# Kernel tuning notes

Hardware: AMD Instinct MI355X
Metric: run time of the kernel (lower is better)

The kernel has to match this reference:

```python
import jax, jax.numpy as jnp
import numpy as np

B_SZ, SEQ, IN, HID, MEM_D, ORDER = 64, 512, 512, 1024, 8, 256
THETA = 512.0


def _legendre_ab(order, theta):
    # Continuous-time Legendre delay system (Voelker et al.):
    # A[i,j] = (2i+1)/theta * (-1 if i<j else (-1)^(i-j+1));  B[i] = (2i+1)/theta * (-1)^i
    q = jnp.arange(order, dtype=jnp.float32)
    r = (2.0 * q + 1.0) / theta
    i, j = jnp.meshgrid(q, q, indexing='ij')
    a = jnp.where(i < j, -1.0, jnp.where(((i - j) % 2) == 1, 1.0, -1.0)) * r[:, None]
    b = jnp.where((q % 2) == 0, 1.0, -1.0) * r
    # ZOH discretization with dt=1 via augmented matrix exponential
    M = jnp.zeros((order + 1, order + 1), dtype=jnp.float32)
    M = M.at[:order, :order].set(a).at[:order, order].set(b)
    Md = jax.scipy.linalg.expm(M)
    return Md[:order, :order], Md[:order, order]


def setup_inputs() -> dict:
    key = jax.random.key(0)
    ks = jax.random.split(key, 7)
    def n(k, shape, s):
        return jax.random.normal(k, shape, dtype=jnp.float32) * jnp.float32(s)
    return {
        'x':   n(ks[0], (B_SZ, SEQ, IN), 1.0),
        'e_x': n(ks[1], (MEM_D, IN), 1.0 / np.sqrt(IN)),          # lecun_uniform_-like scale
        'e_h': n(ks[2], (MEM_D, HID), 1.0 / np.sqrt(HID)),
        'e_m': jnp.zeros((MEM_D, MEM_D * ORDER), dtype=jnp.float32),  # init_em = zeros_
        'W_x': n(ks[4], (HID, IN), np.sqrt(2.0 / (HID + IN))),    # xavier_normal_
        'W_h': n(ks[5], (HID, HID), np.sqrt(2.0 / (HID + HID))),
        'W_m': n(ks[6], (HID, MEM_D * ORDER), np.sqrt(2.0 / (HID + MEM_D * ORDER))),
    }


def reference(x, e_x, e_h, e_m, W_x, W_h, W_m):
    A, Bv = _legendre_ab(ORDER, THETA)
    bsz = x.shape[0]

    def step(carry, x_t):
        h, m = carry                      # h: [B,HID], m: [B,MEM_D,ORDER]
        m_flat = m.reshape(bsz, -1)
        # u_t = e_x x_t + e_h h_{t-1} + e_m m_{t-1}  -> [B, MEM_D]
        u = x_t @ e_x.T + h @ e_h.T + m_flat @ e_m.T
        # m_t = A m_{t-1} + B u_t (per memory channel)
        m = jnp.einsum('bdo,po->bdp', m, A) + u[:, :, None] * Bv
        m_flat = m.reshape(bsz, -1)
        # h_t = tanh(W_x x_t + W_h h_{t-1} + W_m m_t)
        h = jnp.tanh(x_t @ W_x.T + h @ W_h.T + m_flat @ W_m.T)
        return (h, m), h

    h0 = jnp.zeros((bsz, HID), dtype=x.dtype)
    m0 = jnp.zeros((bsz, MEM_D, ORDER), dtype=x.dtype)
    (_, _), ys = jax.lax.scan(step, (h0, m0), jnp.swapaxes(x, 0, 1))
    return jnp.swapaxes(ys, 0, 1)          # [B, SEQ, HID]
```

## Files before the change

### kernel.cpp

```cpp
#include <hip/hip_runtime.h>
#include <cmath>
#include <vector>

#define B_SZ 64
#define SEQ 512
#define IN_D 512
#define HID 1024
#define MEM_DIM 8
#define ORD 256
#define MFLAT 2048
#define KTOT 3584
#define NH 128
#define NM 64
#define NBLK (NH + NM)

typedef __attribute__((ext_vector_type(8))) short short8v;
typedef __attribute__((ext_vector_type(4))) float f32x4;

__device__ __host__ inline unsigned short f2bf(float f) {
  union { float f; unsigned u; } v; v.f = f;
  unsigned r = v.u + 0x7FFF + ((v.u >> 16) & 1);
  return (unsigned short)(r >> 16);
}
__device__ __host__ inline float bf2f(unsigned short h) {
  union { unsigned u; float f; } v; v.u = ((unsigned)h) << 16;
  return v.f;
}

static void matmul_d(const double* A, const double* B, double* C, int n) {
  for (int i = 0; i < n; ++i) {
    double* Ci = C + (size_t)i * n;
    for (int j = 0; j < n; ++j) Ci[j] = 0.0;
    const double* Ai = A + (size_t)i * n;
    for (int k = 0; k < n; ++k) {
      double a = Ai[k];
      const double* Bk = B + (size_t)k * n;
      for (int j = 0; j < n; ++j) Ci[j] += a * Bk[j];
    }
  }
}

static void compute_AB_host(float* AdT, float* Anat, float* Bd) {
  const int q = ORD, n = ORD + 1;
  const double theta = 512.0;
  std::vector<double> M((size_t)n * n, 0.0);
  for (int i = 0; i < q; ++i) {
    double r = (2.0 * i + 1.0) / theta;
    for (int j = 0; j < q; ++j) {
      double v = (i < j) ? -1.0 : ((((i - j) % 2) == 1) ? 1.0 : -1.0);
      M[(size_t)i * n + j] = v * r;
    }
    M[(size_t)i * n + q] = (((i % 2) == 0) ? 1.0 : -1.0) * r;
  }
  double norm = 0.0;
  for (int j = 0; j < n; ++j) {
    double s = 0.0;
    for (int i = 0; i < n; ++i) s += fabs(M[(size_t)i * n + j]);
    if (s > norm) norm = s;
  }
  int s = 0;
  while (norm > 0.25) { norm *= 0.5; ++s; }
  double sc = ldexp(1.0, -s);
  for (size_t i = 0; i < M.size(); ++i) M[i] *= sc;
  std::vector<double> E((size_t)n * n, 0.0), P = M, T((size_t)n * n);
  for (int i = 0; i < n; ++i) E[(size_t)i * n + i] = 1.0;
  for (size_t i = 0; i < M.size(); ++i) E[i] += M[i];
  for (int k = 2; k <= 30; ++k) {
    matmul_d(P.data(), M.data(), T.data(), n);
    double inv = 1.0 / (double)k, mx = 0.0;
    for (size_t i = 0; i < T.size(); ++i) {
      T[i] *= inv;
      double a = fabs(T[i]);
      if (a > mx) mx = a;
    }
    P.swap(T);
    for (size_t i = 0; i < M.size(); ++i) E[i] += P[i];
    if (mx < 1e-19) break;
  }
  for (int it = 0; it < s; ++it) {
    matmul_d(E.data(), E.data(), T.data(), n);
    E.swap(T);
  }
  for (int p = 0; p < q; ++p) {
    for (int o = 0; o < q; ++o) {
      float v = (float)E[(size_t)p * n + o];
      AdT[(size_t)o * q + p] = v;
      Anat[(size_t)p * q + o] = v;
    }
    Bd[p] = (float)E[(size_t)p * n + q];
  }
}

__global__ __launch_bounds__(256) void k_wmb(const float* __restrict__ Wm,
                                             const float* __restrict__ Bd,
                                             float* __restrict__ WmB) {
  int i = blockIdx.x;
  int d = threadIdx.x >> 5, l = threadIdx.x & 31;
  const float* wr = Wm + (size_t)i * MFLAT + d * ORD;
  float acc = 0.f;
  #pragma unroll
  for (int j = 0; j < 8; ++j) { int p = l + 32 * j; acc += wr[p] * Bd[p]; }
  for (int off = 16; off; off >>= 1) acc += __shfl_xor(acc, off);
  if (l == 0) WmB[i * 8 + d] = acc;
}

__global__ __launch_bounds__(256) void k_gcat(
    const float* __restrict__ Wx, const float* __restrict__ Wh,
    const float* __restrict__ Wm, const float* __restrict__ Ex,
    const float* __restrict__ Eh, const float* __restrict__ Em,
    const float* __restrict__ Anat, const float* __restrict__ WmB,
    unsigned short* __restrict__ Ghi, unsigned short* __restrict__ Glo) {
  __shared__ float wm[MFLAT];
  __shared__ float wb[8];
  int i = blockIdx.x, tid = threadIdx.x;
  for (int k = tid; k < MFLAT; k += 256) wm[k] = Wm[(size_t)i * MFLAT + k];
  if (tid < 8) wb[tid] = WmB[i * 8 + tid];
  __syncthreads();
  unsigned short* grh = Ghi + (size_t)i * KTOT;
  unsigned short* grl = Glo + (size_t)i * KTOT;
  for (int c = tid; c < KTOT; c += 256) {
    float v;
    if (c < IN_D) {
      v = Wx[(size_t)i * IN_D + c];
      #pragma unroll
      for (int d = 0; d < 8; ++d) v += wb[d] * Ex[(size_t)d * IN_D + c];
    } else if (c < IN_D + HID) {
      int j = c - IN_D;
      v = Wh[(size_t)i * HID + j];
      #pragma unroll
      for (int d = 0; d < 8; ++d) v += wb[d] * Eh[(size_t)d * HID + j];
    } else {
      int cm = c - IN_D - HID;
      int dd = cm >> 8, o = cm & 255;
      v = 0.f;
      const float* wmd = wm + dd * ORD;
      for (int p = 0; p < ORD; ++p) v += wmd[p] * Anat[(size_t)p * ORD + o];
      #pragma unroll
      for (int d = 0; d < 8; ++d) v += wb[d] * Em[(size_t)d * MFLAT + cm];
    }
    unsigned short hi = f2bf(v);
    grh[c] = hi;
    grl[c] = f2bf(v - bf2f(hi));
  }
}

__device__ inline void grid_barrier(unsigned* cnt, unsigned target) {
  __syncthreads();
  if (threadIdx.x == 0) {
    __hip_atomic_fetch_add(cnt, 1u, __ATOMIC_RELEASE, __HIP_MEMORY_SCOPE_AGENT);
    while (__hip_atomic_load(cnt, __ATOMIC_RELAXED, __HIP_MEMORY_SCOPE_AGENT) < target)
      __builtin_amdgcn_s_sleep(1);
    __builtin_amdgcn_fence(__ATOMIC_ACQUIRE, "agent");
  }
  __syncthreads();
}

__global__ __launch_bounds__(256) void k_persist(
    const float* __restrict__ x, const float* __restrict__ Ex,
    const float* __restrict__ Eh, const float* __restrict__ Em,
    const unsigned short* __restrict__ Ghi, const unsigned short* __restrict__ Glo,
    const float* __restrict__ AdT, const float* __restrict__ Bd,
    unsigned short* __restrict__ sh0, unsigned short* __restrict__ sh1,
    unsigned short* __restrict__ sl0, unsigned short* __restrict__ sl1,
    float* __restrict__ hfp0, float* __restrict__ hfp1,
    float* __restrict__ mfp0, float* __restrict__ mfp1,
    float* __restrict__ out, unsigned* __restrict__ cnt) {
  int tid = threadIdx.x;
  unsigned ep = 0;

  if (blockIdx.x < NH) {
    __shared__ float hx[2][64][4];
    int it = blockIdx.x & 63, bh = blockIdx.x >> 6;
    int w = tid >> 6, lane = tid & 63;
    int tw = w & 1, kh = w >> 1;
    int b0 = bh * 32 + tw * 16;
    int i0 = it * 16;
    size_t aoff = (size_t)(b0 + (lane & 15)) * KTOT + (lane >> 4) * 8;
    const unsigned short* bh_ = Ghi + (size_t)(i0 + (lane & 15)) * KTOT + (lane >> 4) * 8;
    const unsigned short* bl_ = Glo + (size_t)(i0 + (lane & 15)) * KTOT + (lane >> 4) * 8;

    grid_barrier(cnt, (++ep) * NBLK);

    for (int t = 0; t < SEQ; ++t) {
      const unsigned short* ah_ = ((t & 1) ? sh1 : sh0) + aoff;
      const unsigned short* al_ = ((t & 1) ? sl1 : sl0) + aoff;
      unsigned short* snh = (t & 1) ? sh0 : sh1;
      unsigned short* snl = (t & 1) ? sl0 : sl1;
      float* hn = (t & 1) ? hfp0 : hfp1;

      f32x4 ahh = {0.f,0.f,0.f,0.f}, alh = {0.f,0.f,0.f,0.f}, ahl = {0.f,0.f,0.f,0.f};
      int kbase = kh * 1792;
      #pragma unroll 4
      for (int kk = 0; kk < 56; ++kk) {
        int k = kbase + kk * 32;
        short8v avh = *(const short8v*)(ah_ + k);
        short8v avl = *(const short8v*)(al_ + k);
        short8v bvh = *(const short8v*)(bh_ + k);
        short8v bvl = *(const short8v*)(bl_ + k);
        ahh = __builtin_amdgcn_mfma_f32_16x16x32_bf16(avh, bvh, ahh, 0, 0, 0);
        alh = __builtin_amdgcn_mfma_f32_16x16x32_bf16(avl, bvh, alh, 0, 0, 0);
        ahl = __builtin_amdgcn_mfma_f32_16x16x32_bf16(avh, bvl, ahl, 0, 0, 0);
      }
      f32x4 acc = ahh + alh + ahl;
      if (kh == 1) {
        *(f32x4*)&hx[tw][lane][0] = acc;
      }
      __syncthreads();
      if (kh == 0) {
        f32x4 o4 = *(const f32x4*)&hx[tw][lane][0];
        #pragma unroll
        for (int r = 0; r < 4; ++r) {
          float v = acc[r] + o4[r];
          float hv = tanhf(v);
          int b = b0 + (lane >> 4) * 4 + r;
          int i = i0 + (lane & 15);
          hn[(size_t)b * HID + i] = hv;
          unsigned short hi = f2bf(hv);
          snh[(size_t)b * KTOT + IN_D + i] = hi;
          snl[(size_t)b * KTOT + IN_D + i] = f2bf(hv - bf2f(hi));
          __builtin_nontemporal_store(hv, &out[((size_t)b * SEQ + t) * HID + i]);
        }
      }
      grid_barrier(cnt, (++ep) * NBLK);
    }
  } else {
    __shared__ float sst[KTOT];
    int b = blockIdx.x - NH;
    int d = tid >> 5, l = tid & 31;
    int p0 = l * 8;
    const float* exr = Ex + (size_t)d * IN_D;
    const float* ehr = Eh + (size_t)d * HID;
    const float* emr = Em + (size_t)d * MFLAT;
    float bdv[8];
    #pragma unroll
    for (int j = 0; j < 8; ++j) bdv[j] = Bd[p0 + j];

    {
      const float* xr = x + (size_t)b * SEQ * IN_D;
      for (int k = tid; k < IN_D; k += 256) {
        float xv = xr[k];
        unsigned short hi = f2bf(xv);
        sh0[(size_t)b * KTOT + k] = hi;
        sl0[(size_t)b * KTOT + k] = f2bf(xv - bf2f(hi));
      }
    }
    grid_barrier(cnt, (++ep) * NBLK);

    for (int t = 0; t < SEQ; ++t) {
      const float* hc = (t & 1) ? hfp1 : hfp0;
      const float* mc = (t & 1) ? mfp1 : mfp0;
      float* mn = (t & 1) ? mfp0 : mfp1;
      unsigned short* snh = (t & 1) ? sh0 : sh1;
      unsigned short* snl = (t & 1) ? sl0 : sl1;

      const float* xrow = x + ((size_t)b * SEQ + t) * IN_D;
      #pragma unroll
      for (int j = 0; j < 14; ++j) {
        int k = tid + 256 * j;
        float v;
        if (k < IN_D) v = xrow[k];
        else if (k < IN_D + HID) v = hc[(size_t)b * HID + (k - IN_D)];
        else v = mc[(size_t)b * MFLAT + (k - IN_D - HID)];
        sst[k] = v;
      }
      __syncthreads();

      float ua = 0.f;
      #pragma unroll 4
      for (int j = 0; j < 16; ++j) { int k = l + 32 * j; ua += exr[k] * sst[k]; }
      #pragma unroll 4
      for (int j = 0; j < 32; ++j) { int k = l + 32 * j; ua += ehr[k] * sst[IN_D + k]; }
      #pragma unroll 4
      for (int j = 0; j < 64; ++j) { int k = l + 32 * j; ua += emr[k] * sst[IN_D + HID + k]; }
      #pragma unroll
      for (int off = 16; off; off >>= 1) ua += __shfl_xor(ua, off);

      float a0 = bdv[0]*ua, a1 = bdv[1]*ua, a2 = bdv[2]*ua, a3 = bdv[3]*ua;
      float a4 = bdv[4]*ua, a5 = bdv[5]*ua, a6 = bdv[6]*ua, a7 = bdv[7]*ua;
      const float* mrow = sst + IN_D + HID + d * ORD;
      #pragma unroll 4
      for (int o = 0; o < ORD; ++o) {
        float mv = mrow[o];
        const float4* aq = (const float4*)(AdT + (size_t)o * ORD + p0);
        float4 q0 = aq[0], q1 = aq[1];
        a0 = fmaf(q0.x, mv, a0); a1 = fmaf(q0.y, mv, a1);
        a2 = fmaf(q0.z, mv, a2); a3 = fmaf(q0.w, mv, a3);
        a4 = fmaf(q1.x, mv, a4); a5 = fmaf(q1.y, mv, a5);
        a6 = fmaf(q1.z, mv, a6); a7 = fmaf(q1.w, mv, a7);
      }
      float4* mo4 = (float4*)(mn + (size_t)b * MFLAT + d * ORD + p0);
      mo4[0] = make_float4(a0, a1, a2, a3);
      mo4[1] = make_float4(a4, a5, a6, a7);
      float av[8] = { a0, a1, a2, a3, a4, a5, a6, a7 };
      unsigned short ph[8], pl[8];
      #pragma unroll
      for (int j = 0; j < 8; ++j) {
        ph[j] = f2bf(av[j]);
        pl[j] = f2bf(av[j] - bf2f(ph[j]));
      }
      size_t moff = (size_t)b * KTOT + IN_D + HID + d * ORD + p0;
      *(short8v*)(snh + moff) = *(short8v*)ph;
      *(short8v*)(snl + moff) = *(short8v*)pl;

      if (t + 1 < SEQ) {
        const float* xn = x + ((size_t)b * SEQ + t + 1) * IN_D;
        for (int k = tid; k < IN_D; k += 256) {
          float xv = xn[k];
          unsigned short hi = f2bf(xv);
          snh[(size_t)b * KTOT + k] = hi;
          snl[(size_t)b * KTOT + k] = f2bf(xv - bf2f(hi));
        }
      }
      __syncthreads();
      grid_barrier(cnt, (++ep) * NBLK);
    }
  }
}

extern "C" void kernel_launch(void* const* d_in, const int* in_sizes, int n_in,
                              void* d_out, int out_size, void* d_ws, size_t ws_size,
                              hipStream_t stream) {
  const float* x  = (const float*)d_in[0];
  const float* Ex = (const float*)d_in[1];
  const float* Eh = (const float*)d_in[2];
  const float* Em = (const float*)d_in[3];
  const float* Wx = (const float*)d_in[4];
  const float* Wh = (const float*)d_in[5];
  const float* Wm = (const float*)d_in[6];
  float* out = (float*)d_out;
  float* ws = (float*)d_ws;

  float* dAnat = ws;
  float* dAdT  = dAnat + 65536;
  float* dBd   = dAdT + 65536;
  float* dWmB  = dBd + 512;
  unsigned short* dGhi = (unsigned short*)(dWmB + 8192);
  unsigned short* dGlo = dGhi + (size_t)HID * KTOT;
  unsigned short* sh0  = dGlo + (size_t)HID * KTOT;
  unsigned short* sh1  = sh0 + (size_t)B_SZ * KTOT;
  unsigned short* sl0  = sh1 + (size_t)B_SZ * KTOT;
  unsigned short* sl1  = sl0 + (size_t)B_SZ * KTOT;
  float* hfp0 = (float*)(sl1 + (size_t)B_SZ * KTOT);
  float* hfp1 = hfp0 + B_SZ * HID;
  float* mfp0 = hfp1 + B_SZ * HID;
  float* mfp1 = mfp0 + B_SZ * MFLAT;
  unsigned* dCnt = (unsigned*)(mfp1 + B_SZ * MFLAT);

  static float h_AdT[ORD * ORD];
  static float h_Anat[ORD * ORD];
  static float h_Bd[ORD];
  compute_AB_host(h_AdT, h_Anat, h_Bd);
  hipMemcpyAsync(dAdT,  h_AdT,  sizeof(h_AdT),  hipMemcpyHostToDevice, stream);
  hipMemcpyAsync(dAnat, h_Anat, sizeof(h_Anat), hipMemcpyHostToDevice, stream);
  hipMemcpyAsync(dBd,   h_Bd,   sizeof(h_Bd),   hipMemcpyHostToDevice, stream);

  hipMemsetAsync(sh0, 0, (size_t)B_SZ * KTOT * sizeof(unsigned short), stream);
  hipMemsetAsync(sl0, 0, (size_t)B_SZ * KTOT * sizeof(unsigned short), stream);
  hipMemsetAsync(hfp0, 0, (size_t)B_SZ * HID * sizeof(float), stream);
  hipMemsetAsync(mfp0, 0, (size_t)B_SZ * MFLAT * sizeof(float), stream);
  hipMemsetAsync(dCnt, 0, sizeof(unsigned), stream);

  k_wmb<<<dim3(HID), dim3(256), 0, stream>>>(Wm, dBd, dWmB);
  k_gcat<<<dim3(HID), dim3(256), 0, stream>>>(Wx, Wh, Wm, Ex, Eh, Em, dAnat, dWmB, dGhi, dGlo);

  k_persist<<<dim3(NBLK), dim3(256), 0, stream>>>(
      x, Ex, Eh, Em, dGhi, dGlo, dAdT, dBd, sh0, sh1, sl0, sl1,
      hfp0, hfp1, mfp0, mfp1, out, dCnt);
}
```

Before: 21.12 ms.

## Replace atomic-counter grid barrier with flag-array barrier and restructure memory update

Swaps the single atomic-counter grid barrier for a centralized scheme. Each block writes its epoch to its own padded flag slot, block 0 polls all the slots, and it then releases everyone through one go flag, so blocks no longer contend on one atomic. The memory-update blocks also change how they compute A·m. Each thread now covers all 8 memory channels for 4 outputs over a quarter of the order dimension, so every AdT element loaded is reused 8 times, and the partial sums are reduced through shared memory. The added cost is extra shared memory, more syncthreads, and a serial poll in block 0 on every step.

```diff
diff --git a/kernel.cpp b/kernel.cpp
--- a/kernel.cpp
+++ b/kernel.cpp
@@ -13,6 +13,7 @@
 #define NH 128
 #define NM 64
 #define NBLK (NH + NM)
+#define BAR_STRIDE 16
 
 typedef __attribute__((ext_vector_type(8))) short short8v;
 typedef __attribute__((ext_vector_type(4))) float f32x4;
@@ -144,14 +145,28 @@
   }
 }
 
-__device__ inline void grid_barrier(unsigned* cnt, unsigned target) {
+__device__ inline void grid_barrier(unsigned* __restrict__ arr,
+                                    unsigned* __restrict__ go, unsigned ep) {
   __syncthreads();
-  if (threadIdx.x == 0) {
-    __hip_atomic_fetch_add(cnt, 1u, __ATOMIC_RELEASE, __HIP_MEMORY_SCOPE_AGENT);
-    while (__hip_atomic_load(cnt, __ATOMIC_RELAXED, __HIP_MEMORY_SCOPE_AGENT) < target)
-      __builtin_amdgcn_s_sleep(1);
+  if (blockIdx.x == 0) {
+    int tid = threadIdx.x;
+    if (tid > 0 && tid < NBLK) {
+      while (__hip_atomic_load(&arr[tid * BAR_STRIDE], __ATOMIC_RELAXED,
+                               __HIP_MEMORY_SCOPE_AGENT) < ep) {}
+    }
+    __syncthreads();
+    if (tid == 0)
+      __hip_atomic_store(go, ep, __ATOMIC_RELEASE, __HIP_MEMORY_SCOPE_AGENT);
+  } else {
+    if (threadIdx.x == 0) {
+      __hip_atomic_store(&arr[blockIdx.x * BAR_STRIDE], ep, __ATOMIC_RELEASE,
+                         __HIP_MEMORY_SCOPE_AGENT);
+      while (__hip_atomic_load(go, __ATOMIC_RELAXED,
+                               __HIP_MEMORY_SCOPE_AGENT) < ep) {}
+    }
+  }
+  if (threadIdx.x == 0)
     __builtin_amdgcn_fence(__ATOMIC_ACQUIRE, "agent");
-  }
   __syncthreads();
 }
 
@@ -164,7 +179,8 @@
     unsigned short* __restrict__ sl0, unsigned short* __restrict__ sl1,
     float* __restrict__ hfp0, float* __restrict__ hfp1,
     float* __restrict__ mfp0, float* __restrict__ mfp1,
-    float* __restrict__ out, unsigned* __restrict__ cnt) {
+    float* __restrict__ out, unsigned* __restrict__ barArr,
+    unsigned* __restrict__ barGo) {
   int tid = threadIdx.x;
   unsigned ep = 0;
 
@@ -179,7 +195,7 @@
     const unsigned short* bh_ = Ghi + (size_t)(i0 + (lane & 15)) * KTOT + (lane >> 4) * 8;
     const unsigned short* bl_ = Glo + (size_t)(i0 + (lane & 15)) * KTOT + (lane >> 4) * 8;
 
-    grid_barrier(cnt, (++ep) * NBLK);
+    grid_barrier(barArr, barGo, ++ep);
 
     for (int t = 0; t < SEQ; ++t) {
       const unsigned short* ah_ = ((t & 1) ? sh1 : sh0) + aoff;
@@ -221,19 +237,24 @@
           __builtin_nontemporal_store(hv, &out[((size_t)b * SEQ + t) * HID + i]);
         }
       }
-      grid_barrier(cnt, (++ep) * NBLK);
+      grid_barrier(barArr, barGo, ++ep);
     }
   } else {
     __shared__ float sst[KTOT];
+    __shared__ float part[4][MFLAT];
+    __shared__ float ush[8];
     int b = blockIdx.x - NH;
-    int d = tid >> 5, l = tid & 31;
-    int p0 = l * 8;
-    const float* exr = Ex + (size_t)d * IN_D;
-    const float* ehr = Eh + (size_t)d * HID;
-    const float* emr = Em + (size_t)d * MFLAT;
+    int du = tid >> 5, lu = tid & 31;
+    const float* exr = Ex + (size_t)du * IN_D;
+    const float* ehr = Eh + (size_t)du * HID;
+    const float* emr = Em + (size_t)du * MFLAT;
+    int os = tid >> 6;
+    int p0 = (tid & 63) * 4;
+    int dp0 = tid * 8;
+    int dr = tid >> 5;
     float bdv[8];
     #pragma unroll
-    for (int j = 0; j < 8; ++j) bdv[j] = Bd[p0 + j];
+    for (int j = 0; j < 8; ++j) bdv[j] = Bd[(dp0 & 255) + j];
 
     {
       const float* xr = x + (size_t)b * SEQ * IN_D;
@@ -244,7 +265,7 @@
         sl0[(size_t)b * KTOT + k] = f2bf(xv - bf2f(hi));
       }
     }
-    grid_barrier(cnt, (++ep) * NBLK);
+    grid_barrier(barArr, barGo, ++ep);
 
     for (int t = 0; t < SEQ; ++t) {
       const float* hc = (t & 1) ? hfp1 : hfp0;
@@ -267,38 +288,61 @@
 
       float ua = 0.f;
       #pragma unroll 4
-      for (int j = 0; j < 16; ++j) { int k = l + 32 * j; ua += exr[k] * sst[k]; }
+      for (int j = 0; j < 16; ++j) { int k = lu + 32 * j; ua += exr[k] * sst[k]; }
       #pragma unroll 4
-      for (int j = 0; j < 32; ++j) { int k = l + 32 * j; ua += ehr[k] * sst[IN_D + k]; }
+      for (int j = 0; j < 32; ++j) { int k = lu + 32 * j; ua += ehr[k] * sst[IN_D + k]; }
       #pragma unroll 4
-      for (int j = 0; j < 64; ++j) { int k = l + 32 * j; ua += emr[k] * sst[IN_D + HID + k]; }
+      for (int j = 0; j < 64; ++j) { int k = lu + 32 * j; ua += emr[k] * sst[IN_D + HID + k]; }
       #pragma unroll
       for (int off = 16; off; off >>= 1) ua += __shfl_xor(ua, off);
-
-      float a0 = bdv[0]*ua, a1 = bdv[1]*ua, a2 = bdv[2]*ua, a3 = bdv[3]*ua;
-      float a4 = bdv[4]*ua, a5 = bdv[5]*ua, a6 = bdv[6]*ua, a7 = bdv[7]*ua;
-      const float* mrow = sst + IN_D + HID + d * ORD;
+      if (lu == 0) ush[du] = ua;
+      __syncthreads();
+
+      float acc[8][4];
+      #pragma unroll
+      for (int d = 0; d < 8; ++d)
+        acc[d][0] = acc[d][1] = acc[d][2] = acc[d][3] = 0.f;
+      const float* mbase = sst + IN_D + HID;
       #pragma unroll 4
-      for (int o = 0; o < ORD; ++o) {
-        float mv = mrow[o];
-        const float4* aq = (const float4*)(AdT + (size_t)o * ORD + p0);
-        float4 q0 = aq[0], q1 = aq[1];
-        a0 = fmaf(q0.x, mv, a0); a1 = fmaf(q0.y, mv, a1);
-        a2 = fmaf(q0.z, mv, a2); a3 = fmaf(q0.w, mv, a3);
-        a4 = fmaf(q1.x, mv, a4); a5 = fmaf(q1.y, mv, a5);
-        a6 = fmaf(q1.z, mv, a6); a7 = fmaf(q1.w, mv, a7);
-      }
-      float4* mo4 = (float4*)(mn + (size_t)b * MFLAT + d * ORD + p0);
-      mo4[0] = make_float4(a0, a1, a2, a3);
-      mo4[1] = make_float4(a4, a5, a6, a7);
-      float av[8] = { a0, a1, a2, a3, a4, a5, a6, a7 };
+      for (int oo = 0; oo < 64; ++oo) {
+        int o = os * 64 + oo;
+        float4 q = *(const float4*)(AdT + (size_t)o * ORD + p0);
+        #pragma unroll
+        for (int d = 0; d < 8; ++d) {
+          float mv = mbase[d * ORD + o];
+          acc[d][0] = fmaf(q.x, mv, acc[d][0]);
+          acc[d][1] = fmaf(q.y, mv, acc[d][1]);
+          acc[d][2] = fmaf(q.z, mv, acc[d][2]);
+          acc[d][3] = fmaf(q.w, mv, acc[d][3]);
+        }
+      }
+      #pragma unroll
+      for (int d = 0; d < 8; ++d)
+        *(float4*)&part[os][d * ORD + p0] =
+            make_float4(acc[d][0], acc[d][1], acc[d][2], acc[d][3]);
+      __syncthreads();
+
+      float r[8];
+      float uv = ush[dr];
+      #pragma unroll
+      for (int j = 0; j < 8; ++j) r[j] = bdv[j] * uv;
+      #pragma unroll
+      for (int s = 0; s < 4; ++s) {
+        float4 v0 = *(const float4*)&part[s][dp0];
+        float4 v1 = *(const float4*)&part[s][dp0 + 4];
+        r[0] += v0.x; r[1] += v0.y; r[2] += v0.z; r[3] += v0.w;
+        r[4] += v1.x; r[5] += v1.y; r[6] += v1.z; r[7] += v1.w;
+      }
+      float4* mo4 = (float4*)(mn + (size_t)b * MFLAT + dp0);
+      mo4[0] = make_float4(r[0], r[1], r[2], r[3]);
+      mo4[1] = make_float4(r[4], r[5], r[6], r[7]);
       unsigned short ph[8], pl[8];
       #pragma unroll
       for (int j = 0; j < 8; ++j) {
-        ph[j] = f2bf(av[j]);
-        pl[j] = f2bf(av[j] - bf2f(ph[j]));
-      }
-      size_t moff = (size_t)b * KTOT + IN_D + HID + d * ORD + p0;
+        ph[j] = f2bf(r[j]);
+        pl[j] = f2bf(r[j] - bf2f(ph[j]));
+      }
+      size_t moff = (size_t)b * KTOT + IN_D + HID + dp0;
       *(short8v*)(snh + moff) = *(short8v*)ph;
       *(short8v*)(snl + moff) = *(short8v*)pl;
 
@@ -311,8 +355,7 @@
           snl[(size_t)b * KTOT + k] = f2bf(xv - bf2f(hi));
         }
       }
-      __syncthreads();
-      grid_barrier(cnt, (++ep) * NBLK);
+      grid_barrier(barArr, barGo, ++ep);
     }
   }
 }
@@ -344,7 +387,8 @@
   float* hfp1 = hfp0 + B_SZ * HID;
   float* mfp0 = hfp1 + B_SZ * HID;
   float* mfp1 = mfp0 + B_SZ * MFLAT;
-  unsigned* dCnt = (unsigned*)(mfp1 + B_SZ * MFLAT);
+  unsigned* barArr = (unsigned*)(mfp1 + B_SZ * MFLAT);
+  unsigned* barGo  = barArr + NBLK * BAR_STRIDE;
 
   static float h_AdT[ORD * ORD];
   static float h_Anat[ORD * ORD];
@@ -358,12 +402,12 @@
   hipMemsetAsync(sl0, 0, (size_t)B_SZ * KTOT * sizeof(unsigned short), stream);
   hipMemsetAsync(hfp0, 0, (size_t)B_SZ * HID * sizeof(float), stream);
   hipMemsetAsync(mfp0, 0, (size_t)B_SZ * MFLAT * sizeof(float), stream);
-  hipMemsetAsync(dCnt, 0, sizeof(unsigned), stream);
+  hipMemsetAsync(barArr, 0, (NBLK * BAR_STRIDE + 16) * sizeof(unsigned), stream);
 
   k_wmb<<<dim3(HID), dim3(256), 0, stream>>>(Wm, dBd, dWmB);
   k_gcat<<<dim3(HID), dim3(256), 0, stream>>>(Wx, Wh, Wm, Ex, Eh, Em, dAnat, dWmB, dGhi, dGlo);
 
   k_persist<<<dim3(NBLK), dim3(256), 0, stream>>>(
       x, Ex, Eh, Em, dGhi, dGlo, dAdT, dBd, sh0, sh1, sl0, sl1,
-      hfp0, hfp1, mfp0, mfp1, out, dCnt);
-}
+      hfp0, hfp1, mfp0, mfp1, out, barArr, barGo);
+}
```

Measured after the change: 19.41 ms. -8.1%, faster.
